# Kernel optimization log

Hardware: AMD Instinct MI355X
Metric: run time of the kernel (lower is better)

The kernel has to match this reference:

```python
import jax, jax.numpy as jnp
import numpy as np

HID = 64        # hid_size
NUM_LAYER = 3
NG = 16         # number of graphs in batch
NPG = 160       # nodes per graph
N = NG * NPG    # 2560 total nodes
DEG = 16
EPG = NPG * DEG # edges per graph
E = NG * EPG    # 40960 total edges
P = NG * NPG * NPG  # 409600 total (i,j) pairs from triu_indices(n, -n)
AV = 64         # atom feature vocab per column (9 columns)
BV = 8          # bond feature vocab per column (3 columns)
EPS = 1e-5


def setup_inputs() -> dict:
    rng = np.random.default_rng(0)
    key = jax.random.key(0)
    ks = jax.random.split(key, 16)

    # categorical node / edge features
    x = jnp.asarray(rng.integers(0, AV, size=(N, 9)), dtype=jnp.int32)
    edge_attr = jnp.asarray(rng.integers(0, BV, size=(E, 3)), dtype=jnp.int32)

    # within-graph random edges (sorted order not required for the math here)
    src_l = rng.integers(0, NPG, size=(NG, EPG))
    dst_l = rng.integers(0, NPG, size=(NG, EPG))
    gid = np.repeat(np.arange(NG), EPG)
    # flat position of edge (u,v) of graph g inside the concatenated all-pairs list
    epos = jnp.asarray(gid * NPG * NPG + src_l.reshape(-1) * NPG + dst_l.reshape(-1),
                       dtype=jnp.int32)

    # idx = concat([triu_indices(n, -n) + ptr[g]]) -> all pairs, row-major per graph
    g = np.arange(NG)[:, None, None]
    i = np.arange(NPG)[None, :, None]
    j = np.arange(NPG)[None, None, :]
    idx0 = jnp.asarray(np.broadcast_to(g * NPG + i, (NG, NPG, NPG)).reshape(-1).astype(np.int32))
    idx1 = jnp.asarray(np.broadcast_to(g * NPG + j, (NG, NPG, NPG)).reshape(-1).astype(np.int32))

    def lin(k, fan_in, fan_out):
        b = 1.0 / np.sqrt(fan_in)
        kw, kb = jax.random.split(k)
        return (jax.random.uniform(kw, (fan_in, fan_out), jnp.float32, -b, b),
                jax.random.uniform(kb, (fan_out,), jnp.float32, -b, b))

    atom_tables = jax.random.normal(ks[0], (9, AV, HID), jnp.float32) * 0.02
    bond_tables = jax.random.normal(ks[1], (3, BV, HID), jnp.float32) * 0.02
    W1, b1 = lin(ks[2], HID, HID)
    W2, b2 = lin(ks[3], HID, HID)
    We, be = lin(ks[4], HID, HID)
    L0_w, L0_b = lin(ks[5], 3 * HID, HID)
    L1_w, L1_b = lin(ks[6], HID, HID)
    L2_w, L2_b = lin(ks[7], HID, 1)
    g0 = jnp.ones((HID,), jnp.float32); beta0 = jnp.zeros((HID,), jnp.float32)
    g1 = jnp.ones((HID,), jnp.float32); beta1 = jnp.zeros((HID,), jnp.float32)

    return dict(atom_tables=atom_tables, bond_tables=bond_tables,
                W1=W1, b1=b1, W2=W2, b2=b2, We=We, be=be,
                L0_w=L0_w, L0_b=L0_b, L1_w=L1_w, L1_b=L1_b, L2_w=L2_w, L2_b=L2_b,
                g0=g0, beta0=beta0, g1=g1, beta1=beta1,
                x=x, edge_attr=edge_attr, idx0=idx0, idx1=idx1, epos=epos)


def _batchnorm(h, gamma, beta):
    mu = jnp.mean(h, axis=0)
    var = jnp.mean(jnp.square(h - mu), axis=0)  # biased var, torch training mode
    return (h - mu) * jax.lax.rsqrt(var + EPS) * gamma + beta


def reference(atom_tables, bond_tables, W1, b1, W2, b2, We, be,
              L0_w, L0_b, L1_w, L1_b, L2_w, L2_b,
              g0, beta0, g1, beta1,
              x, edge_attr, idx0, idx1, epos):
    # AtomEncoder / BondEncoder: sum of per-column embedding lookups
    cols9 = jnp.arange(9)[None, :]
    x_emb = atom_tables[cols9, x].sum(axis=1)          # [N, HID]
    cols3 = jnp.arange(3)[None, :]
    ea_emb = bond_tables[cols3, edge_attr].sum(axis=1)  # [E, HID]

    n1 = (x_emb @ W1 + b1)[idx0]                        # [P, HID]
    n2 = (x_emb @ W2 + b2)[idx1]                        # [P, HID]

    e = ea_emb @ We + be                                # [E, HID]
    # equivalent of SparseTensor.to_dense()[idx0, idx1] without the N^2 dense blowup;
    # duplicate edges sum, missing pairs are zero (matches to_dense semantics)
    e_pairs = jnp.zeros((P, HID), e.dtype).at[epos].add(e)

    emb = jnp.concatenate((n1, n2, e_pairs), axis=-1)   # [P, 3*HID]

    emb = jax.nn.relu(_batchnorm(emb @ L0_w + L0_b, g0, beta0))
    emb = jax.nn.relu(_batchnorm(emb @ L1_w + L1_b, g1, beta1))
    emb = emb @ L2_w + L2_b                             # [P, 1]
    return jnp.squeeze(emb, axis=-1)                    # [P]
```

## Files before the change

### kernel.cpp

```cpp
#include <hip/hip_runtime.h>
#include <hip/hip_bf16.h>

#define HID 64
#define NGr 16
#define NPG 160
#define NN  2560
#define EE  40960
#define PPG 25600
#define PT  409600
#define AV  64
#define BV  8
#define EPSB 1e-5f

__global__ void k_prep(const float* __restrict__ W1, const float* __restrict__ b1,
                       const float* __restrict__ W2, const float* __restrict__ b2,
                       const float* __restrict__ We, const float* __restrict__ be,
                       const float* __restrict__ L0w, const float* __restrict__ L0b,
                       float* __restrict__ W1c, float* __restrict__ W2c, float* __restrict__ Wec,
                       float* __restrict__ b1c, float* __restrict__ b2c, float* __restrict__ bec,
                       float* __restrict__ stats) {
    int blk = blockIdx.x, tid = threadIdx.x;
    if (blk == 3) { stats[tid] = 0.f; return; }
    const float* Wsrc = (blk == 0) ? W1 : (blk == 1) ? W2 : We;
    const float* bsrc = (blk == 0) ? b1 : (blk == 1) ? b2 : be;
    const float* L    = L0w + blk * 64 * 64;
    float* Wdst = (blk == 0) ? W1c : (blk == 1) ? W2c : Wec;
    float* bdst = (blk == 0) ? b1c : (blk == 1) ? b2c : bec;
    for (int idx = tid; idx < 4096; idx += 256) {
        int k = idx >> 6, h = idx & 63;
        float acc = 0.f;
        for (int m = 0; m < 64; ++m) acc = fmaf(Wsrc[k * 64 + m], L[m * 64 + h], acc);
        Wdst[idx] = acc;
    }
    if (tid < 64) {
        int h = tid;
        float acc = (blk == 0) ? L0b[h] : 0.f;
        for (int m = 0; m < 64; ++m) acc = fmaf(bsrc[m], L[m * 64 + h], acc);
        bdst[h] = acc;
    }
}

__global__ void k_nodes(const float* __restrict__ atab, const int* __restrict__ x,
                        const float* __restrict__ W1c, const float* __restrict__ W2c,
                        const float* __restrict__ b1c, const float* __restrict__ b2c,
                        float* __restrict__ A, float* __restrict__ Bm) {
    int n = blockIdx.x, h = threadIdx.x;
    __shared__ float xe[64];
    float v = 0.f;
#pragma unroll
    for (int c = 0; c < 9; ++c) v += atab[c * AV * HID + x[n * 9 + c] * HID + h];
    xe[h] = v;
    __syncthreads();
    float a = b1c[h], b = b2c[h];
#pragma unroll
    for (int k = 0; k < 64; ++k) {
        float xk = xe[k];
        a = fmaf(xk, W1c[k * 64 + h], a);
        b = fmaf(xk, W2c[k * 64 + h], b);
    }
    A[n * 64 + h] = a;
    Bm[n * 64 + h] = b;
}

__global__ void __launch_bounds__(256) k_dense(const float* __restrict__ A, const float* __restrict__ Bm,
                                               float* __restrict__ zbuf, float* __restrict__ stats) {
    int h = threadIdx.x & 63;
    int wid = threadIdx.x >> 6;
    int wavesTotal = gridDim.x * 4;
    int wave = blockIdx.x * 4 + wid;
    float s = 0.f, ss = 0.f;
    for (int row = wave; row < PT; row += wavesTotal) {
        int g = row / PPG;
        int rem = row - g * PPG;
        int i = rem / NPG;
        int j = rem - i * NPG;
        float v = A[(g * NPG + i) * 64 + h] + Bm[(g * NPG + j) * 64 + h];
        zbuf[(size_t)row * 64 + h] = v;
        s += v;
        ss = fmaf(v, v, ss);
    }
    __shared__ float ls[128];
    if (threadIdx.x < 128) ls[threadIdx.x] = 0.f;
    __syncthreads();
    atomicAdd(&ls[h], s);
    atomicAdd(&ls[64 + h], ss);
    __syncthreads();
    if (threadIdx.x < 128) atomicAdd(&stats[threadIdx.x], ls[threadIdx.x]);
}

__global__ void __launch_bounds__(256) k_edges(const float* __restrict__ btab, const int* __restrict__ eattr,
                                               const int* __restrict__ epos,
                                               const float* __restrict__ Wec, const float* __restrict__ bec,
                                               float* __restrict__ zbuf, float* __restrict__ stats) {
    int h = threadIdx.x & 63;
    int el = threadIdx.x >> 6;
    __shared__ float ea[4][64];
    float s = 0.f, ss = 0.f;
    for (int base = blockIdx.x * 4; base < EE; base += gridDim.x * 4) {
        int e = base + el;
        float v = 0.f;
#pragma unroll
        for (int c = 0; c < 3; ++c) v += btab[c * BV * HID + eattr[e * 3 + c] * HID + h];
        ea[el][h] = v;
        __syncthreads();
        float ew = bec[h];
#pragma unroll
        for (int k = 0; k < 64; ++k) ew = fmaf(ea[el][k], Wec[k * 64 + h], ew);
        int p = epos[e];
        float old = atomicAdd(&zbuf[(size_t)p * 64 + h], ew);
        s += ew;
        ss += 2.f * old * ew + ew * ew;
        __syncthreads();
    }
    __shared__ float ls[128];
    if (threadIdx.x < 128) ls[threadIdx.x] = 0.f;
    __syncthreads();
    atomicAdd(&ls[h], s);
    atomicAdd(&ls[64 + h], ss);
    __syncthreads();
    if (threadIdx.x < 128) atomicAdd(&stats[threadIdx.x], ls[threadIdx.x]);
}

__global__ void __launch_bounds__(256) k_mid(const float* __restrict__ L1w, const float* __restrict__ L1b,
                                             const float* __restrict__ g0, const float* __restrict__ beta0,
                                             float* __restrict__ zbuf, float* __restrict__ stats) {
    int h = threadIdx.x & 63;
    int wid = threadIdx.x >> 6;
    const float invP = 1.f / (float)PT;
    float mu = stats[h] * invP;
    float var = stats[64 + h] * invP - mu * mu;
    float inv = rsqrtf(var + EPSB);
    float s0 = g0[h] * inv;
    float t0 = fmaf(-mu, s0, beta0[h]);
    float w[64];
#pragma unroll
    for (int k = 0; k < 64; ++k) w[k] = L1w[k * 64 + h];
    float bias = L1b[h];
    int wavesTotal = gridDim.x * 4;
    int stride = wavesTotal;
    int row = blockIdx.x * 4 + wid;
    float s = 0.f, ss = 0.f;
    if (row < PT) {
        float z = zbuf[(size_t)row * 64 + h];
        while (true) {
            int nrow = row + stride;
            float znext = (nrow < PT) ? zbuf[(size_t)nrow * 64 + h] : 0.f;
            float h0 = fmaxf(fmaf(z, s0, t0), 0.f);
            int h0b = __float_as_int(h0);
            float a0 = bias, a1 = 0.f, a2 = 0.f, a3 = 0.f;
#pragma unroll
            for (int k = 0; k < 64; k += 4) {
                a0 = fmaf(__int_as_float(__builtin_amdgcn_readlane(h0b, k)),     w[k],     a0);
                a1 = fmaf(__int_as_float(__builtin_amdgcn_readlane(h0b, k + 1)), w[k + 1], a1);
                a2 = fmaf(__int_as_float(__builtin_amdgcn_readlane(h0b, k + 2)), w[k + 2], a2);
                a3 = fmaf(__int_as_float(__builtin_amdgcn_readlane(h0b, k + 3)), w[k + 3], a3);
            }
            float z1 = (a0 + a1) + (a2 + a3);
            zbuf[(size_t)row * 64 + h] = z1;
            s += z1;
            ss = fmaf(z1, z1, ss);
            if (nrow >= PT) break;
            row = nrow;
            z = znext;
        }
    }
    __shared__ float ls[128];
    if (threadIdx.x < 128) ls[threadIdx.x] = 0.f;
    __syncthreads();
    atomicAdd(&ls[h], s);
    atomicAdd(&ls[64 + h], ss);
    __syncthreads();
    if (threadIdx.x < 128) atomicAdd(&stats[128 + threadIdx.x], ls[threadIdx.x]);
}

__global__ void __launch_bounds__(256) k_final(const float* __restrict__ g1, const float* __restrict__ beta1,
                                               const float* __restrict__ L2w, const float* __restrict__ L2b,
                                               const float* __restrict__ zbuf, float* __restrict__ out,
                                               const float* __restrict__ stats) {
    int lane = threadIdx.x & 63;
    int wid = threadIdx.x >> 6;
    int q = lane & 15;
    int rl = lane >> 4;
    const float invP = 1.f / (float)PT;
    float s1[4], t1[4], wv[4];
#pragma unroll
    for (int c = 0; c < 4; ++c) {
        int col = q * 4 + c;
        float mu = stats[128 + col] * invP;
        float var = stats[192 + col] * invP - mu * mu;
        float inv = rsqrtf(var + EPSB);
        s1[c] = g1[col] * inv;
        t1[c] = fmaf(-mu, s1[c], beta1[col]);
        wv[c] = L2w[col];
    }
    float bias = L2b[0];
    int waveId = blockIdx.x * 4 + wid;
    int stride = gridDim.x * 16;
    for (int base = waveId * 4; base < PT; base += stride) {
        const float4 zv = *reinterpret_cast<const float4*>(zbuf + (size_t)base * 64 + lane * 4);
        float p;
        p  = fmaxf(fmaf(zv.x, s1[0], t1[0]), 0.f) * wv[0];
        p  = fmaf(fmaxf(fmaf(zv.y, s1[1], t1[1]), 0.f), wv[1], p);
        p  = fmaf(fmaxf(fmaf(zv.z, s1[2], t1[2]), 0.f), wv[2], p);
        p  = fmaf(fmaxf(fmaf(zv.w, s1[3], t1[3]), 0.f), wv[3], p);
        p += __shfl_xor(p, 1);
        p += __shfl_xor(p, 2);
        p += __shfl_xor(p, 4);
        p += __shfl_xor(p, 8);
        if (q == 0) out[base + rl] = p + bias;
    }
}

extern "C" void kernel_launch(void* const* d_in, const int* in_sizes, int n_in,
                              void* d_out, int out_size, void* d_ws, size_t ws_size,
                              hipStream_t stream) {
    const float* atab  = (const float*)d_in[0];
    const float* btab  = (const float*)d_in[1];
    const float* W1    = (const float*)d_in[2];
    const float* b1    = (const float*)d_in[3];
    const float* W2    = (const float*)d_in[4];
    const float* b2    = (const float*)d_in[5];
    const float* We    = (const float*)d_in[6];
    const float* be    = (const float*)d_in[7];
    const float* L0w   = (const float*)d_in[8];
    const float* L0b   = (const float*)d_in[9];
    const float* L1w   = (const float*)d_in[10];
    const float* L1b   = (const float*)d_in[11];
    const float* L2w   = (const float*)d_in[12];
    const float* L2b   = (const float*)d_in[13];
    const float* g0    = (const float*)d_in[14];
    const float* beta0 = (const float*)d_in[15];
    const float* g1    = (const float*)d_in[16];
    const float* beta1 = (const float*)d_in[17];
    const int*   x     = (const int*)d_in[18];
    const int*   eattr = (const int*)d_in[19];
    const int*   epos  = (const int*)d_in[22];
    float* out = (float*)d_out;

    float* ws = (float*)d_ws;
    float* zbuf = ws;
    float* A    = zbuf + (size_t)PT * 64;
    float* Bm   = A + NN * 64;
    float* W1c  = Bm + NN * 64;
    float* W2c  = W1c + 4096;
    float* Wec  = W2c + 4096;
    float* b1c  = Wec + 4096;
    float* b2c  = b1c + 64;
    float* bec  = b2c + 64;
    float* stats = bec + 64;

    k_prep<<<4, 256, 0, stream>>>(W1, b1, W2, b2, We, be, L0w, L0b,
                                  W1c, W2c, Wec, b1c, b2c, bec, stats);
    k_nodes<<<NN, 64, 0, stream>>>(atab, x, W1c, W2c, b1c, b2c, A, Bm);
    k_dense<<<2048, 256, 0, stream>>>(A, Bm, zbuf, stats);
    k_edges<<<512, 256, 0, stream>>>(btab, eattr, epos, Wec, bec, zbuf, stats);
    k_mid<<<2048, 256, 0, stream>>>(L1w, L1b, g0, beta0, zbuf, stats);
    k_final<<<1024, 256, 0, stream>>>(g1, beta1, L2w, L2b, zbuf, out, stats);
}
```

Measured before the change: 252.6 us.

## Run layer-1 linear on MFMA with split-bf16 precision compensation

```diff
diff --git a/kernel.cpp b/kernel.cpp
--- a/kernel.cpp
+++ b/kernel.cpp
@@ -12,15 +12,37 @@
 #define BV  8
 #define EPSB 1e-5f
 
+typedef __attribute__((ext_vector_type(8))) short short8v;
+typedef __attribute__((ext_vector_type(4))) float f32x4;
+
+static __device__ __forceinline__ unsigned short bf16_hi(float v) {
+    return (unsigned short)(__float_as_uint(v) >> 16);
+}
+static __device__ __forceinline__ float bf16_val(unsigned short h) {
+    return __uint_as_float(((unsigned int)h) << 16);
+}
+
 __global__ void k_prep(const float* __restrict__ W1, const float* __restrict__ b1,
                        const float* __restrict__ W2, const float* __restrict__ b2,
                        const float* __restrict__ We, const float* __restrict__ be,
                        const float* __restrict__ L0w, const float* __restrict__ L0b,
+                       const float* __restrict__ L1w,
                        float* __restrict__ W1c, float* __restrict__ W2c, float* __restrict__ Wec,
                        float* __restrict__ b1c, float* __restrict__ b2c, float* __restrict__ bec,
-                       float* __restrict__ stats) {
+                       float* __restrict__ stats,
+                       unsigned short* __restrict__ WBhi, unsigned short* __restrict__ WBlo) {
     int blk = blockIdx.x, tid = threadIdx.x;
-    if (blk == 3) { stats[tid] = 0.f; return; }
+    if (blk == 3) {
+        stats[tid] = 0.f;
+        for (int idx = tid; idx < 4096; idx += 256) {
+            float w = L1w[idx];
+            unsigned short hi = bf16_hi(w);
+            float rem = w - bf16_val(hi);
+            WBhi[idx] = hi;
+            WBlo[idx] = bf16_hi(rem);
+        }
+        return;
+    }
     const float* Wsrc = (blk == 0) ? W1 : (blk == 1) ? W2 : We;
     const float* bsrc = (blk == 0) ? b1 : (blk == 1) ? b2 : be;
     const float* L    = L0w + blk * 64 * 64;
@@ -121,56 +143,110 @@
     if (threadIdx.x < 128) atomicAdd(&stats[threadIdx.x], ls[threadIdx.x]);
 }
 
-__global__ void __launch_bounds__(256) k_mid(const float* __restrict__ L1w, const float* __restrict__ L1b,
+__global__ void __launch_bounds__(256) k_mid(const unsigned short* __restrict__ WBhi,
+                                             const unsigned short* __restrict__ WBlo,
+                                             const float* __restrict__ L1b,
                                              const float* __restrict__ g0, const float* __restrict__ beta0,
                                              float* __restrict__ zbuf, float* __restrict__ stats) {
-    int h = threadIdx.x & 63;
-    int wid = threadIdx.x >> 6;
+    int lane = threadIdx.x & 63;
+    int wid  = blockIdx.x * 4 + (threadIdx.x >> 6);
+    int nWaves = gridDim.x * 4;
+    int r16 = lane & 15;
+    int kg  = lane >> 4;
+
     const float invP = 1.f / (float)PT;
-    float mu = stats[h] * invP;
-    float var = stats[64 + h] * invP - mu * mu;
-    float inv = rsqrtf(var + EPSB);
-    float s0 = g0[h] * inv;
-    float t0 = fmaf(-mu, s0, beta0[h]);
-    float w[64];
-#pragma unroll
-    for (int k = 0; k < 64; ++k) w[k] = L1w[k * 64 + h];
-    float bias = L1b[h];
-    int wavesTotal = gridDim.x * 4;
-    int stride = wavesTotal;
-    int row = blockIdx.x * 4 + wid;
-    float s = 0.f, ss = 0.f;
-    if (row < PT) {
-        float z = zbuf[(size_t)row * 64 + h];
-        while (true) {
-            int nrow = row + stride;
-            float znext = (nrow < PT) ? zbuf[(size_t)nrow * 64 + h] : 0.f;
-            float h0 = fmaxf(fmaf(z, s0, t0), 0.f);
-            int h0b = __float_as_int(h0);
-            float a0 = bias, a1 = 0.f, a2 = 0.f, a3 = 0.f;
-#pragma unroll
-            for (int k = 0; k < 64; k += 4) {
-                a0 = fmaf(__int_as_float(__builtin_amdgcn_readlane(h0b, k)),     w[k],     a0);
-                a1 = fmaf(__int_as_float(__builtin_amdgcn_readlane(h0b, k + 1)), w[k + 1], a1);
-                a2 = fmaf(__int_as_float(__builtin_amdgcn_readlane(h0b, k + 2)), w[k + 2], a2);
-                a3 = fmaf(__int_as_float(__builtin_amdgcn_readlane(h0b, k + 3)), w[k + 3], a3);
+    float s0a[8], t0a[8], s0b[8], t0b[8];
+#pragma unroll
+    for (int j = 0; j < 8; ++j) {
+        int k = kg * 8 + j;
+        float mu = stats[k] * invP;
+        float var = stats[64 + k] * invP - mu * mu;
+        float inv = rsqrtf(var + EPSB);
+        s0a[j] = g0[k] * inv;
+        t0a[j] = fmaf(-mu, s0a[j], beta0[k]);
+        int k2 = k + 32;
+        float mu2 = stats[k2] * invP;
+        float var2 = stats[64 + k2] * invP - mu2 * mu2;
+        float inv2 = rsqrtf(var2 + EPSB);
+        s0b[j] = g0[k2] * inv2;
+        t0b[j] = fmaf(-mu2, s0b[j], beta0[k2]);
+    }
+    short8v Bhi[4][2], Blo[4][2];
+#pragma unroll
+    for (int ct = 0; ct < 4; ++ct)
+#pragma unroll
+        for (int ks = 0; ks < 2; ++ks)
+#pragma unroll
+            for (int j = 0; j < 8; ++j) {
+                int k = ks * 32 + kg * 8 + j;
+                int idx = k * 64 + ct * 16 + r16;
+                Bhi[ct][ks][j] = (short)WBhi[idx];
+                Blo[ct][ks][j] = (short)WBlo[idx];
             }
-            float z1 = (a0 + a1) + (a2 + a3);
-            zbuf[(size_t)row * 64 + h] = z1;
-            s += z1;
-            ss = fmaf(z1, z1, ss);
-            if (nrow >= PT) break;
-            row = nrow;
-            z = znext;
-        }
-    }
-    __shared__ float ls[128];
-    if (threadIdx.x < 128) ls[threadIdx.x] = 0.f;
-    __syncthreads();
-    atomicAdd(&ls[h], s);
-    atomicAdd(&ls[64 + h], ss);
-    __syncthreads();
-    if (threadIdx.x < 128) atomicAdd(&stats[128 + threadIdx.x], ls[threadIdx.x]);
+    float biasv[4];
+#pragma unroll
+    for (int ct = 0; ct < 4; ++ct) biasv[ct] = L1b[ct * 16 + r16];
+
+    float sum[4] = {0.f, 0.f, 0.f, 0.f}, ssum[4] = {0.f, 0.f, 0.f, 0.f};
+
+    for (int tile = wid; tile < PT / 16; tile += nWaves) {
+        float* tb = zbuf + (size_t)tile * 16 * 64;
+        const float4 za0 = *reinterpret_cast<const float4*>(tb + r16 * 64 + kg * 8);
+        const float4 za1 = *reinterpret_cast<const float4*>(tb + r16 * 64 + kg * 8 + 4);
+        const float4 zb0 = *reinterpret_cast<const float4*>(tb + r16 * 64 + 32 + kg * 8);
+        const float4 zb1 = *reinterpret_cast<const float4*>(tb + r16 * 64 + 32 + kg * 8 + 4);
+        float ha[8] = {za0.x, za0.y, za0.z, za0.w, za1.x, za1.y, za1.z, za1.w};
+        float hb[8] = {zb0.x, zb0.y, zb0.z, zb0.w, zb1.x, zb1.y, zb1.z, zb1.w};
+        short8v aHi0, aLo0, aHi1, aLo1;
+#pragma unroll
+        for (int j = 0; j < 8; ++j) {
+            float hv = fmaxf(fmaf(ha[j], s0a[j], t0a[j]), 0.f);
+            unsigned short hi = bf16_hi(hv);
+            float rem = hv - bf16_val(hi);
+            aHi0[j] = (short)hi;
+            aLo0[j] = (short)bf16_hi(rem);
+            float hv2 = fmaxf(fmaf(hb[j], s0b[j], t0b[j]), 0.f);
+            unsigned short hi2 = bf16_hi(hv2);
+            float rem2 = hv2 - bf16_val(hi2);
+            aHi1[j] = (short)hi2;
+            aLo1[j] = (short)bf16_hi(rem2);
+        }
+        f32x4 acc[4];
+#pragma unroll
+        for (int ct = 0; ct < 4; ++ct) acc[ct] = (f32x4){0.f, 0.f, 0.f, 0.f};
+#pragma unroll
+        for (int ct = 0; ct < 4; ++ct) {
+            acc[ct] = __builtin_amdgcn_mfma_f32_16x16x32_bf16(aHi0, Bhi[ct][0], acc[ct], 0, 0, 0);
+            acc[ct] = __builtin_amdgcn_mfma_f32_16x16x32_bf16(aHi0, Blo[ct][0], acc[ct], 0, 0, 0);
+            acc[ct] = __builtin_amdgcn_mfma_f32_16x16x32_bf16(aLo0, Bhi[ct][0], acc[ct], 0, 0, 0);
+            acc[ct] = __builtin_amdgcn_mfma_f32_16x16x32_bf16(aHi1, Bhi[ct][1], acc[ct], 0, 0, 0);
+            acc[ct] = __builtin_amdgcn_mfma_f32_16x16x32_bf16(aHi1, Blo[ct][1], acc[ct], 0, 0, 0);
+            acc[ct] = __builtin_amdgcn_mfma_f32_16x16x32_bf16(aLo1, Bhi[ct][1], acc[ct], 0, 0, 0);
+        }
+#pragma unroll
+        for (int ct = 0; ct < 4; ++ct) {
+#pragma unroll
+            for (int reg = 0; reg < 4; ++reg) {
+                float z = acc[ct][reg] + biasv[ct];
+                tb[(kg * 4 + reg) * 64 + ct * 16 + r16] = z;
+                sum[ct] += z;
+                ssum[ct] = fmaf(z, z, ssum[ct]);
+            }
+        }
+    }
+#pragma unroll
+    for (int ct = 0; ct < 4; ++ct) {
+        float s = sum[ct];
+        s += __shfl_xor(s, 16);
+        s += __shfl_xor(s, 32);
+        float q = ssum[ct];
+        q += __shfl_xor(q, 16);
+        q += __shfl_xor(q, 32);
+        if (kg == 0) {
+            atomicAdd(&stats[128 + ct * 16 + r16], s);
+            atomicAdd(&stats[192 + ct * 16 + r16], q);
+        }
+    }
 }
 
 __global__ void __launch_bounds__(256) k_final(const float* __restrict__ g1, const float* __restrict__ beta1,
@@ -248,12 +324,14 @@
     float* b2c  = b1c + 64;
     float* bec  = b2c + 64;
     float* stats = bec + 64;
-
-    k_prep<<<4, 256, 0, stream>>>(W1, b1, W2, b2, We, be, L0w, L0b,
-                                  W1c, W2c, Wec, b1c, b2c, bec, stats);
+    unsigned short* WBhi = (unsigned short*)(stats + 256);
+    unsigned short* WBlo = WBhi + 4096;
+
+    k_prep<<<4, 256, 0, stream>>>(W1, b1, W2, b2, We, be, L0w, L0b, L1w,
+                                  W1c, W2c, Wec, b1c, b2c, bec, stats, WBhi, WBlo);
     k_nodes<<<NN, 64, 0, stream>>>(atab, x, W1c, W2c, b1c, b2c, A, Bm);
     k_dense<<<2048, 256, 0, stream>>>(A, Bm, zbuf, stats);
     k_edges<<<512, 256, 0, stream>>>(btab, eattr, epos, Wec, bec, zbuf, stats);
-    k_mid<<<2048, 256, 0, stream>>>(L1w, L1b, g0, beta0, zbuf, stats);
+    k_mid<<<512, 256, 0, stream>>>(WBhi, WBlo, L1b, g0, beta0, zbuf, stats);
     k_final<<<1024, 256, 0, stream>>>(g1, beta1, L2w, L2b, zbuf, out, stats);
 }
```

After: 231.4 us. 8.4% less time.
